# Kernel optimization log

Measured on AMD Instinct MI355X. Metric: run time of the kernel, lower is better.

## Reference

```python
import jax, jax.numpy as jnp
import numpy as np

CUTOFF = 5.0
N_ENV = 8
F0, F1 = 16, 32  # filter_dims
D = 256          # feature_dim


def setup_inputs() -> dict:
    key = jax.random.key(0)
    ks = jax.random.split(key, 12)
    B, E, N = 128, 64, 32
    r = jax.random.normal(ks[0], (B, E, 3), jnp.float32) * 3.0
    # neighbors placed near r so distances fall inside the cutoff
    r_nb = r[..., None, :] + jax.random.normal(ks[1], (B, E, N, 3), jnp.float32) * 1.5
    ee_scales = jax.random.uniform(ks[2], (N_ENV,), jnp.float32, 0.5, CUTOFF)
    ee_kernel = jax.random.normal(ks[3], (4, F0), jnp.float32) / jnp.sqrt(4.0)
    ee_bias = jax.random.normal(ks[4], (F0,), jnp.float32) * 2.0
    beta_kernel = jax.random.normal(ks[5], (F0 + N_ENV, F1), jnp.float32) / jnp.sqrt(F0 + N_ENV + 0.0)
    beta_bias = jnp.zeros((F1,), jnp.float32)
    gamma_kernel = jax.random.normal(ks[6], (F1, D), jnp.float32) / jnp.sqrt(F1 + 0.0)
    dense1_kernel = jax.random.normal(ks[7], (4, D), jnp.float32) / jnp.sqrt(4.0)
    dense1_bias = jnp.zeros((D,), jnp.float32)
    out_kernel = jax.random.normal(ks[8], (D, D), jnp.float32) / jnp.sqrt(D + 0.0)
    out_bias = jnp.zeros((D,), jnp.float32)
    return dict(r=r, r_nb=r_nb, ee_scales=ee_scales, ee_kernel=ee_kernel, ee_bias=ee_bias,
                beta_kernel=beta_kernel, beta_bias=beta_bias, gamma_kernel=gamma_kernel,
                dense1_kernel=dense1_kernel, dense1_bias=dense1_bias,
                out_kernel=out_kernel, out_bias=out_bias)


def reference(r, r_nb, ee_scales, ee_kernel, ee_bias, beta_kernel, beta_bias,
              gamma_kernel, dense1_kernel, dense1_bias, out_kernel, out_bias):
    # pairwise diff features: [dist, dx, dy, dz] per neighbor
    diff = r_nb - r[..., None, :]                       # [B,E,N,3]
    dist = jnp.linalg.norm(diff, axis=-1, keepdims=True)  # [B,E,N,1]
    feats = jnp.concatenate([dist, diff], axis=-1)      # [B,E,N,4]

    # PairwiseFilter (beta_ee): envelopes + small dense, gated by smooth cutoff
    env = jnp.exp(-jnp.square(dist / ee_scales))        # [B,E,N,N_ENV]
    h = jnp.tanh(feats @ ee_kernel + ee_bias)           # [B,E,N,F0]
    x = dist / CUTOFF
    fcut = jnp.where(x < 1.0, 0.5 * (jnp.cos(jnp.pi * x) + 1.0), 0.0)
    beta = (jnp.concatenate([h, env], axis=-1) @ beta_kernel + beta_bias) * fcut  # [B,E,N,F1]

    gamma = beta @ gamma_kernel                         # [B,E,N,D]

    # rescale features: first column (dist) becomes log1p(dist)
    inp = feats / dist * jnp.log1p(dist)                # [B,E,N,4]
    feat = jax.nn.silu(inp @ dense1_kernel + dense1_bias)  # [B,E,N,D]

    res = jnp.einsum('...id,...id->...d', feat, gamma)  # sum over neighbors -> [B,E,D]
    res = jax.nn.silu(res @ out_kernel + out_bias)
    return res
```

## Files before the change

### kernel.cpp

```cpp
#include <hip/hip_runtime.h>
#include <hip/hip_bf16.h>

constexpr int NB   = 32;
constexpr int NENV = 8;
constexpr int F0   = 16;
constexpr int F1   = 32;
constexpr int D    = 256;
constexpr int PAIRS = 128 * 64;
constexpr float CUT = 5.0f;

typedef float f32x4 __attribute__((ext_vector_type(4)));
typedef short s16x8 __attribute__((ext_vector_type(8)));

__device__ __forceinline__ float fast_rcp(float x) { return __builtin_amdgcn_rcpf(x); }
__device__ __forceinline__ float silu(float a) {
  return a * fast_rcp(1.0f + __expf(-a));
}
__device__ __forceinline__ float fast_tanh(float t) {
  return 1.0f - 2.0f * fast_rcp(__expf(2.0f * t) + 1.0f);
}
__device__ __forceinline__ unsigned int cvt_pk_bf16(float a, float b) {
  unsigned int r;
  asm("v_cvt_pk_bf16_f32 %0, %1, %2" : "=v"(r) : "v"(a), "v"(b));
  return r;
}
__device__ __forceinline__ unsigned short f2bf(float f) {
  return (unsigned short)(cvt_pk_bf16(f, f) & 0xffffu);
}

__global__ __launch_bounds__(256)
void moon_fused(
    const float* __restrict__ r,
    const float* __restrict__ r_nb,
    const float* __restrict__ ee_scales,
    const float* __restrict__ ee_kernel,
    const float* __restrict__ ee_bias,
    const float* __restrict__ beta_kernel,
    const float* __restrict__ beta_bias,
    const float* __restrict__ gamma_kernel,
    const float* __restrict__ dense1_kernel,
    const float* __restrict__ dense1_bias,
    const float* __restrict__ out_kernel,
    const float* __restrict__ out_bias,
    float* __restrict__ out)
{
  __shared__ float s_eek[4 * F0];
  __shared__ float s_eeb[F0];
  __shared__ float s_is2[NENV];
  __shared__ unsigned short s_ghT[4][D * 8];
  __shared__ unsigned short s_d1kT[D * 8];
  __shared__ unsigned short s_bkh[4][F1 * 8];
  __shared__ unsigned short s_hb[8][4][NB * 8];
  __shared__ unsigned short s_inph[8][NB * 8];
  __shared__ float s_fcut[8][NB];
  __shared__ unsigned short s_resall[8 * 264];

  const int tid = threadIdx.x;
  const int w   = tid >> 6;
  const int l   = tid & 63;
  const int be0 = blockIdx.x * 8;

  if (tid < 64)       s_eek[tid]      = ee_kernel[tid];
  else if (tid < 80)  s_eeb[tid - 64] = ee_bias[tid - 64];
  else if (tid < 88) { float s = ee_scales[tid - 80]; s_is2[tid - 80] = 1.0f / (s * s); }

  if (tid < 128) {
    const int c = tid & 31;
    const int g = tid >> 5;
    unsigned int q[4];
    if (g < 3) {
      float v[8];
      #pragma unroll
      for (int j = 0; j < 8; ++j) v[j] = beta_kernel[(g * 8 + j) * F1 + c];
      q[0] = cvt_pk_bf16(v[0], v[1]); q[1] = cvt_pk_bf16(v[2], v[3]);
      q[2] = cvt_pk_bf16(v[4], v[5]); q[3] = cvt_pk_bf16(v[6], v[7]);
    } else {
      q[0] = cvt_pk_bf16(beta_bias[c], 0.0f); q[1] = 0; q[2] = 0; q[3] = 0;
    }
    *(uint4*)&s_bkh[g][c * 8] = make_uint4(q[0], q[1], q[2], q[3]);
  }

  {
    const int d = tid;
    unsigned int pk[16];
    #pragma unroll
    for (int k2 = 0; k2 < 16; ++k2)
      pk[k2] = cvt_pk_bf16(gamma_kernel[(2 * k2 + 0) * D + d],
                           gamma_kernel[(2 * k2 + 1) * D + d]);
    #pragma unroll
    for (int g = 0; g < 4; ++g)
      *(uint4*)&s_ghT[g][d * 8] = make_uint4(pk[4*g], pk[4*g+1], pk[4*g+2], pk[4*g+3]);
  }
  {
    const int d = tid;
    unsigned int p0 = cvt_pk_bf16(0.25f * dense1_kernel[0 * D + d],
                                  0.25f * dense1_kernel[1 * D + d]);
    unsigned int p1 = cvt_pk_bf16(0.25f * dense1_kernel[2 * D + d],
                                  0.25f * dense1_kernel[3 * D + d]);
    unsigned int p2 = cvt_pk_bf16(0.25f * dense1_bias[d], 0.0f);
    *(uint4*)&s_d1kT[d * 8] = make_uint4(p0, p1, p2, 0u);
  }

  __syncthreads();

  const int li = l & 15;
  const int g  = l >> 4;

  {
    const int ph = l >> 5;
    const int n  = l & 31;
    const int p  = w * 2 + ph;
    const int bep = be0 + p;
    float rx = r[bep * 3 + 0];
    float ry = r[bep * 3 + 1];
    float rz = r[bep * 3 + 2];
    const float* rn = r_nb + (bep * NB + n) * 3;
    float dx = rn[0] - rx;
    float dy = rn[1] - ry;
    float dz = rn[2] - rz;
    float d2 = dx * dx + dy * dy + dz * dz;
    float dist = sqrtf(d2);
    float feats[4] = {dist, dx, dy, dz};
    float h[16];
    #pragma unroll
    for (int j = 0; j < 16; ++j) {
      float t = s_eeb[j];
      #pragma unroll
      for (int i = 0; i < 4; ++i) t += feats[i] * s_eek[i * F0 + j];
      h[j] = fast_tanh(t);
    }
    unsigned int hp0 = cvt_pk_bf16(h[0], h[1]);
    unsigned int hp1 = cvt_pk_bf16(h[2], h[3]);
    unsigned int hp2 = cvt_pk_bf16(h[4], h[5]);
    unsigned int hp3 = cvt_pk_bf16(h[6], h[7]);
    unsigned int hp4 = cvt_pk_bf16(h[8], h[9]);
    unsigned int hp5 = cvt_pk_bf16(h[10], h[11]);
    unsigned int hp6 = cvt_pk_bf16(h[12], h[13]);
    unsigned int hp7 = cvt_pk_bf16(h[14], h[15]);
    *(uint4*)&s_hb[p][0][n * 8] = make_uint4(hp0, hp1, hp2, hp3);
    *(uint4*)&s_hb[p][1][n * 8] = make_uint4(hp4, hp5, hp6, hp7);
    *(uint4*)&s_hb[p][3][n * 8] = make_uint4(0x3F80u, 0u, 0u, 0u);
    float env[NENV];
    #pragma unroll
    for (int s = 0; s < NENV; ++s) env[s] = __expf(-d2 * s_is2[s]);
    unsigned int e0 = cvt_pk_bf16(env[0], env[1]);
    unsigned int e1 = cvt_pk_bf16(env[2], env[3]);
    unsigned int e2 = cvt_pk_bf16(env[4], env[5]);
    unsigned int e3 = cvt_pk_bf16(env[6], env[7]);
    *(uint4*)&s_hb[p][2][n * 8] = make_uint4(e0, e1, e2, e3);
    float lp  = log1pf(dist);
    float inv = lp / dist;
    unsigned int q0 = cvt_pk_bf16(lp, dx * inv);
    unsigned int q1 = cvt_pk_bf16(dy * inv, dz * inv);
    *(uint4*)&s_inph[p][n * 8] = make_uint4(q0, q1, 0x3F80u, 0u);
    float xc = dist * (1.0f / CUT);
    s_fcut[p][n] = (xc < 1.0f)
                 ? 0.5f * (__cosf(3.14159265358979323846f * xc) + 1.0f)
                 : 0.0f;
  }

  auto beta_pair = [&](int p) {
    s16x8 ah0 = *(const s16x8*)&s_hb[p][g][(0 * 16 + li) * 8];
    s16x8 ah1 = *(const s16x8*)&s_hb[p][g][(1 * 16 + li) * 8];
    s16x8 bb0 = *(const s16x8*)&s_bkh[g][(0 * 16 + li) * 8];
    s16x8 bb1 = *(const s16x8*)&s_bkh[g][(1 * 16 + li) * 8];
    f32x4 z = {0.f, 0.f, 0.f, 0.f};
    f32x4 c00 = __builtin_amdgcn_mfma_f32_16x16x32_bf16(ah0, bb0, z, 0, 0, 0);
    f32x4 c01 = __builtin_amdgcn_mfma_f32_16x16x32_bf16(ah0, bb1, z, 0, 0, 0);
    f32x4 c10 = __builtin_amdgcn_mfma_f32_16x16x32_bf16(ah1, bb0, z, 0, 0, 0);
    f32x4 c11 = __builtin_amdgcn_mfma_f32_16x16x32_bf16(ah1, bb1, z, 0, 0, 0);
    const int cl = li >> 3;
    const int sl = li & 7;
    #pragma unroll
    for (int reg = 0; reg < 4; ++reg) {
      int row0 = g * 4 + reg;
      int row1 = 16 + g * 4 + reg;
      float fc0 = s_fcut[p][row0];
      float fc1 = s_fcut[p][row1];
      s_hb[p][cl    ][row0 * 8 + sl] = f2bf(c00[reg] * fc0);
      s_hb[p][2 + cl][row0 * 8 + sl] = f2bf(c01[reg] * fc0);
      s_hb[p][cl    ][row1 * 8 + sl] = f2bf(c10[reg] * fc1);
      s_hb[p][2 + cl][row1 * 8 + sl] = f2bf(c11[reg] * fc1);
    }
  };
  beta_pair(w * 2 + 0);
  beta_pair(w * 2 + 1);

  auto phase2_pair = [&](int p) {
    s16x8 a0 = *(const s16x8*)&s_hb[p][g][(0 * 16 + li) * 8];
    s16x8 a1 = *(const s16x8*)&s_hb[p][g][(1 * 16 + li) * 8];
    s16x8 ai0 = *(const s16x8*)&s_inph[p][(0 * 16 + li) * 8];
    s16x8 ai1 = *(const s16x8*)&s_inph[p][(1 * 16 + li) * 8];

    #pragma unroll 4
    for (int nt = 0; nt < 16; ++nt) {
      const int d = nt * 16 + li;
      s16x8 b  = *(const s16x8*)&s_ghT[g][d * 8];
      s16x8 bd = *(const s16x8*)&s_d1kT[d * 8];
      f32x4 z = {0.f, 0.f, 0.f, 0.f};
      f32x4 c0 = __builtin_amdgcn_mfma_f32_16x16x32_bf16(a0, b, z, 0, 0, 0);
      f32x4 c1 = __builtin_amdgcn_mfma_f32_16x16x32_bf16(a1, b, z, 0, 0, 0);
      f32x4 f0 = __builtin_amdgcn_mfma_f32_16x16x32_bf16(ai0, bd, z, 0, 0, 0);
      f32x4 f1 = __builtin_amdgcn_mfma_f32_16x16x32_bf16(ai1, bd, z, 0, 0, 0);
      float pv = 0.f;
      #pragma unroll
      for (int reg = 0; reg < 4; ++reg) {
        pv += silu(f0[reg]) * c0[reg];
        pv += silu(f1[reg]) * c1[reg];
      }
      pv += __shfl_xor(pv, 16);
      pv += __shfl_xor(pv, 32);
      if (g == (nt & 3)) s_resall[p * 264 + nt * 16 + li] = f2bf(pv);
    }
  };
  phase2_pair(w * 2 + 0);
  phase2_pair(w * 2 + 1);

  __syncthreads();

  {
    const int col0 = w * 64;
    float bi[4];
    #pragma unroll
    for (int nt = 0; nt < 4; ++nt) bi[nt] = out_bias[col0 + nt * 16 + li];

    f32x4 acc[4] = {{0.f,0.f,0.f,0.f},{0.f,0.f,0.f,0.f},{0.f,0.f,0.f,0.f},{0.f,0.f,0.f,0.f}};
    const unsigned short* arow = &s_resall[(li & 7) * 264 + g * 8];
    const float* wp = out_kernel + col0 + li;

    #pragma unroll 2
    for (int ks = 0; ks < 8; ++ks) {
      s16x8 a = *(const s16x8*)(arow + ks * 32);
      const float* wk0 = wp + (ks * 32 + g * 8) * D;
      #pragma unroll
      for (int nt = 0; nt < 4; ++nt) {
        const float* wq = wk0 + nt * 16;
        union { s16x8 v; unsigned int u[4]; } ub;
        #pragma unroll
        for (int jj = 0; jj < 4; ++jj)
          ub.u[jj] = cvt_pk_bf16(wq[(2 * jj) * D], wq[(2 * jj + 1) * D]);
        acc[nt] = __builtin_amdgcn_mfma_f32_16x16x32_bf16(a, ub.v, acc[nt], 0, 0, 0);
      }
    }
    if (g < 2) {
      #pragma unroll
      for (int nt = 0; nt < 4; ++nt) {
        #pragma unroll
        for (int reg = 0; reg < 4; ++reg) {
          out[(be0 + g * 4 + reg) * D + col0 + nt * 16 + li] = silu(acc[nt][reg] + bi[nt]);
        }
      }
    }
  }
}

extern "C" void kernel_launch(void* const* d_in, const int* in_sizes, int n_in,
                              void* d_out, int out_size, void* d_ws, size_t ws_size,
                              hipStream_t stream) {
  const float* r            = (const float*)d_in[0];
  const float* r_nb         = (const float*)d_in[1];
  const float* ee_scales    = (const float*)d_in[2];
  const float* ee_kernel    = (const float*)d_in[3];
  const float* ee_bias      = (const float*)d_in[4];
  const float* beta_kernel  = (const float*)d_in[5];
  const float* beta_bias    = (const float*)d_in[6];
  const float* gamma_kernel = (const float*)d_in[7];
  const float* dense1_kernel= (const float*)d_in[8];
  const float* dense1_bias  = (const float*)d_in[9];
  const float* out_kernel   = (const float*)d_in[10];
  const float* out_bias     = (const float*)d_in[11];
  float* out = (float*)d_out;
  (void)d_ws; (void)ws_size;

  hipLaunchKernelGGL(moon_fused, dim3(PAIRS / 8), dim3(256), 0, stream,
                     r, r_nb, ee_scales, ee_kernel, ee_bias,
                     beta_kernel, beta_bias, gamma_kernel,
                     dense1_kernel, dense1_bias, out_kernel, out_bias, out);
}
```

Measured before the change: 115.5 us.

## Shrink LDS footprint: keep beta weights and cutoff in registers, alias result buffer

Removes several shared-memory arrays to cut per-block LDS use. The beta kernel fragments are loaded straight from global into registers, and the cutoff factor is passed between lanes with shuffles instead of a shared array. The small ee kernel/bias values are read directly from global memory. The dense1 weights are packed into 3 dwords per column instead of 8 shorts, and the per-pair result rows reuse the s_inph buffer. The aim is to fit more blocks per CU at once, at the cost of extra global loads, shuffles and possible bank conflicts on the split dense1 reads.

```diff
diff --git a/kernel.cpp b/kernel.cpp
--- a/kernel.cpp
+++ b/kernel.cpp
@@ -44,41 +44,19 @@
     const float* __restrict__ out_bias,
     float* __restrict__ out)
 {
-  __shared__ float s_eek[4 * F0];
-  __shared__ float s_eeb[F0];
-  __shared__ float s_is2[NENV];
   __shared__ unsigned short s_ghT[4][D * 8];
-  __shared__ unsigned short s_d1kT[D * 8];
-  __shared__ unsigned short s_bkh[4][F1 * 8];
   __shared__ unsigned short s_hb[8][4][NB * 8];
   __shared__ unsigned short s_inph[8][NB * 8];
-  __shared__ float s_fcut[8][NB];
-  __shared__ unsigned short s_resall[8 * 264];
+  __shared__ unsigned int s_d1a[2 * D];
+  __shared__ unsigned int s_d1b[D];
+  __shared__ float s_is2[NENV];
 
   const int tid = threadIdx.x;
   const int w   = tid >> 6;
   const int l   = tid & 63;
   const int be0 = blockIdx.x * 8;
 
-  if (tid < 64)       s_eek[tid]      = ee_kernel[tid];
-  else if (tid < 80)  s_eeb[tid - 64] = ee_bias[tid - 64];
-  else if (tid < 88) { float s = ee_scales[tid - 80]; s_is2[tid - 80] = 1.0f / (s * s); }
-
-  if (tid < 128) {
-    const int c = tid & 31;
-    const int g = tid >> 5;
-    unsigned int q[4];
-    if (g < 3) {
-      float v[8];
-      #pragma unroll
-      for (int j = 0; j < 8; ++j) v[j] = beta_kernel[(g * 8 + j) * F1 + c];
-      q[0] = cvt_pk_bf16(v[0], v[1]); q[1] = cvt_pk_bf16(v[2], v[3]);
-      q[2] = cvt_pk_bf16(v[4], v[5]); q[3] = cvt_pk_bf16(v[6], v[7]);
-    } else {
-      q[0] = cvt_pk_bf16(beta_bias[c], 0.0f); q[1] = 0; q[2] = 0; q[3] = 0;
-    }
-    *(uint4*)&s_bkh[g][c * 8] = make_uint4(q[0], q[1], q[2], q[3]);
-  }
+  if (tid < 8) { float s = ee_scales[tid]; s_is2[tid] = 1.0f / (s * s); }
 
   {
     const int d = tid;
@@ -98,7 +76,9 @@
     unsigned int p1 = cvt_pk_bf16(0.25f * dense1_kernel[2 * D + d],
                                   0.25f * dense1_kernel[3 * D + d]);
     unsigned int p2 = cvt_pk_bf16(0.25f * dense1_bias[d], 0.0f);
-    *(uint4*)&s_d1kT[d * 8] = make_uint4(p0, p1, p2, 0u);
+    s_d1a[2 * d + 0] = p0;
+    s_d1a[2 * d + 1] = p1;
+    s_d1b[d] = p2;
   }
 
   __syncthreads();
@@ -106,6 +86,7 @@
   const int li = l & 15;
   const int g  = l >> 4;
 
+  float my_fcut;
   {
     const int ph = l >> 5;
     const int n  = l & 31;
@@ -124,9 +105,9 @@
     float h[16];
     #pragma unroll
     for (int j = 0; j < 16; ++j) {
-      float t = s_eeb[j];
-      #pragma unroll
-      for (int i = 0; i < 4; ++i) t += feats[i] * s_eek[i * F0 + j];
+      float t = ee_bias[j];
+      #pragma unroll
+      for (int i = 0; i < 4; ++i) t += feats[i] * ee_kernel[i * F0 + j];
       h[j] = fast_tanh(t);
     }
     unsigned int hp0 = cvt_pk_bf16(h[0], h[1]);
@@ -154,16 +135,31 @@
     unsigned int q1 = cvt_pk_bf16(dy * inv, dz * inv);
     *(uint4*)&s_inph[p][n * 8] = make_uint4(q0, q1, 0x3F80u, 0u);
     float xc = dist * (1.0f / CUT);
-    s_fcut[p][n] = (xc < 1.0f)
-                 ? 0.5f * (__cosf(3.14159265358979323846f * xc) + 1.0f)
-                 : 0.0f;
+    my_fcut = (xc < 1.0f)
+            ? 0.5f * (__cosf(3.14159265358979323846f * xc) + 1.0f)
+            : 0.0f;
+  }
+
+  s16x8 bb0, bb1;
+  {
+    union { s16x8 v; unsigned int u[4]; } u0, u1;
+    if (g < 3) {
+      const float* bk0 = beta_kernel + (g * 8) * F1 + li;
+      #pragma unroll
+      for (int jj = 0; jj < 4; ++jj) {
+        u0.u[jj] = cvt_pk_bf16(bk0[(2 * jj) * F1],      bk0[(2 * jj + 1) * F1]);
+        u1.u[jj] = cvt_pk_bf16(bk0[(2 * jj) * F1 + 16], bk0[(2 * jj + 1) * F1 + 16]);
+      }
+    } else {
+      u0.u[0] = cvt_pk_bf16(beta_bias[li], 0.0f);      u0.u[1] = u0.u[2] = u0.u[3] = 0u;
+      u1.u[0] = cvt_pk_bf16(beta_bias[16 + li], 0.0f); u1.u[1] = u1.u[2] = u1.u[3] = 0u;
+    }
+    bb0 = u0.v; bb1 = u1.v;
   }
 
   auto beta_pair = [&](int p) {
     s16x8 ah0 = *(const s16x8*)&s_hb[p][g][(0 * 16 + li) * 8];
     s16x8 ah1 = *(const s16x8*)&s_hb[p][g][(1 * 16 + li) * 8];
-    s16x8 bb0 = *(const s16x8*)&s_bkh[g][(0 * 16 + li) * 8];
-    s16x8 bb1 = *(const s16x8*)&s_bkh[g][(1 * 16 + li) * 8];
     f32x4 z = {0.f, 0.f, 0.f, 0.f};
     f32x4 c00 = __builtin_amdgcn_mfma_f32_16x16x32_bf16(ah0, bb0, z, 0, 0, 0);
     f32x4 c01 = __builtin_amdgcn_mfma_f32_16x16x32_bf16(ah0, bb1, z, 0, 0, 0);
@@ -171,12 +167,13 @@
     f32x4 c11 = __builtin_amdgcn_mfma_f32_16x16x32_bf16(ah1, bb1, z, 0, 0, 0);
     const int cl = li >> 3;
     const int sl = li & 7;
+    const int base = (p & 1) * 32;
     #pragma unroll
     for (int reg = 0; reg < 4; ++reg) {
       int row0 = g * 4 + reg;
       int row1 = 16 + g * 4 + reg;
-      float fc0 = s_fcut[p][row0];
-      float fc1 = s_fcut[p][row1];
+      float fc0 = __shfl(my_fcut, base + row0);
+      float fc1 = __shfl(my_fcut, base + row1);
       s_hb[p][cl    ][row0 * 8 + sl] = f2bf(c00[reg] * fc0);
       s_hb[p][2 + cl][row0 * 8 + sl] = f2bf(c01[reg] * fc0);
       s_hb[p][cl    ][row1 * 8 + sl] = f2bf(c10[reg] * fc1);
@@ -186,6 +183,7 @@
   beta_pair(w * 2 + 0);
   beta_pair(w * 2 + 1);
 
+  unsigned short* resall = &s_inph[0][0];
   auto phase2_pair = [&](int p) {
     s16x8 a0 = *(const s16x8*)&s_hb[p][g][(0 * 16 + li) * 8];
     s16x8 a1 = *(const s16x8*)&s_hb[p][g][(1 * 16 + li) * 8];
@@ -195,13 +193,17 @@
     #pragma unroll 4
     for (int nt = 0; nt < 16; ++nt) {
       const int d = nt * 16 + li;
-      s16x8 b  = *(const s16x8*)&s_ghT[g][d * 8];
-      s16x8 bd = *(const s16x8*)&s_d1kT[d * 8];
+      s16x8 b = *(const s16x8*)&s_ghT[g][d * 8];
+      union { s16x8 v; unsigned int u[4]; } ud;
+      ud.u[0] = s_d1a[2 * d + 0];
+      ud.u[1] = s_d1a[2 * d + 1];
+      ud.u[2] = s_d1b[d];
+      ud.u[3] = 0u;
       f32x4 z = {0.f, 0.f, 0.f, 0.f};
       f32x4 c0 = __builtin_amdgcn_mfma_f32_16x16x32_bf16(a0, b, z, 0, 0, 0);
       f32x4 c1 = __builtin_amdgcn_mfma_f32_16x16x32_bf16(a1, b, z, 0, 0, 0);
-      f32x4 f0 = __builtin_amdgcn_mfma_f32_16x16x32_bf16(ai0, bd, z, 0, 0, 0);
-      f32x4 f1 = __builtin_amdgcn_mfma_f32_16x16x32_bf16(ai1, bd, z, 0, 0, 0);
+      f32x4 f0 = __builtin_amdgcn_mfma_f32_16x16x32_bf16(ai0, ud.v, z, 0, 0, 0);
+      f32x4 f1 = __builtin_amdgcn_mfma_f32_16x16x32_bf16(ai1, ud.v, z, 0, 0, 0);
       float pv = 0.f;
       #pragma unroll
       for (int reg = 0; reg < 4; ++reg) {
@@ -210,7 +212,7 @@
       }
       pv += __shfl_xor(pv, 16);
       pv += __shfl_xor(pv, 32);
-      if (g == (nt & 3)) s_resall[p * 264 + nt * 16 + li] = f2bf(pv);
+      if (g == (nt & 3)) resall[p * 256 + nt * 16 + li] = f2bf(pv);
     }
   };
   phase2_pair(w * 2 + 0);
@@ -225,7 +227,7 @@
     for (int nt = 0; nt < 4; ++nt) bi[nt] = out_bias[col0 + nt * 16 + li];
 
     f32x4 acc[4] = {{0.f,0.f,0.f,0.f},{0.f,0.f,0.f,0.f},{0.f,0.f,0.f,0.f},{0.f,0.f,0.f,0.f}};
-    const unsigned short* arow = &s_resall[(li & 7) * 264 + g * 8];
+    const unsigned short* arow = resall + (li & 7) * 256 + g * 8;
     const float* wp = out_kernel + col0 + li;
 
     #pragma unroll 2
```

After: 113.4 us. About the same (-1.9%).
